# Optimization experiments

Measured on AMD Instinct MI355X. Metric: run time of the kernel, lower is better.

## Reference

```python
import jax, jax.numpy as jnp
import numpy as np

B, Q, V, H, U = 4, 256, 2048, 512, 128

def setup_inputs() -> dict:
    key = jax.random.key(0)
    ks = jax.random.split(key, 5)
    return {
        "queries": jax.random.normal(ks[0], (B, Q, H), dtype=jnp.float32),
        "values": jax.random.normal(ks[1], (B, V, H), dtype=jnp.float32),
        "w1": jax.random.normal(ks[2], (H, U), dtype=jnp.float32) / np.sqrt(H),
        "w2": jax.random.normal(ks[3], (H, U), dtype=jnp.float32) / np.sqrt(H),
        "v": jax.random.normal(ks[4], (U,), dtype=jnp.float32) / np.sqrt(U),
    }

def reference(queries, values, w1, w2, v):
    # Project queries and values first (cheap GEMMs), then broadcast-add.
    pq = jnp.einsum("bqh,hu->bqu", queries, w1)          # [B,Q,U]
    pv = jnp.einsum("bvh,hu->bvu", values, w2)           # [B,V,U]
    # added_qv: [B,Q,V,U] -- the large intermediate the original materializes
    scores = jnp.einsum("bqvu,u->bqv", jnp.tanh(pq[:, :, None, :] + pv[:, None, :, :]), v)
    attn = jax.nn.softmax(scores, axis=-1)               # softmax over V (last axis, as tf.nn.softmax)
    return jnp.einsum("bqv,bvh->bqh", attn, values)      # [B,Q,H]
```

## Files before the change

kernel.cpp:

```cpp
#include <hip/hip_runtime.h>

#define BB 4
#define QQ 256
#define VV 2048
#define HH 512
#define UU 128

#define C2E   2.8853900817779268f
#define LOG2E 1.4426950408889634f

__device__ __forceinline__ void fma4(float4& a, float s, const float4& w) {
    a.x = fmaf(s, w.x, a.x);
    a.y = fmaf(s, w.y, a.y);
    a.z = fmaf(s, w.z, a.z);
    a.w = fmaf(s, w.w, a.w);
}
__device__ __forceinline__ float2 rcp2(float2 x) {
    return make_float2(__builtin_amdgcn_rcpf(x.x), __builtin_amdgcn_rcpf(x.y));
}
__device__ __forceinline__ float2 mul2(float2 a, float2 b) { return make_float2(a.x*b.x, a.y*b.y); }
__device__ __forceinline__ float2 muls(float2 a, float s)  { return make_float2(a.x*s, a.y*s); }
__device__ __forceinline__ float2 fma2(float2 a, float2 b, float2 c) {
    return make_float2(fmaf(a.x, b.x, c.x), fmaf(a.y, b.y, c.y));
}
__device__ __forceinline__ float2 fmas(float2 a, float s, float2 c) {
    return make_float2(fmaf(a.x, s, c.x), fmaf(a.y, s, c.y));
}

__global__ __launch_bounds__(256) void proj_kernel(const float* __restrict__ queries,
                                                   const float* __restrict__ values,
                                                   const float* __restrict__ w1,
                                                   const float* __restrict__ w2,
                                                   float* __restrict__ pqI,
                                                   float* __restrict__ pvI,
                                                   float* __restrict__ denom) {
    __shared__ float smem[32 * 36 + 32 * 128];
    float (*As)[36] = (float(*)[36])smem;
    float* Ws = smem + 32 * 36;
    float (*Ls)[36] = (float(*)[36])smem;

    const int bid = blockIdx.x;
    const int tid = threadIdx.x;
    if (bid == 0) *(float4*)&denom[tid * 4] = make_float4(0.f, 0.f, 0.f, 0.f);

    const bool isv = (bid < 256);
    const float* A; const float* W; int b, r0, ROWS; float* Ob;
    if (isv) {
        b = bid >> 6; r0 = (bid & 63) * 32;
        A = values + ((size_t)(b * VV + r0)) * HH;  W = w2;
        Ob = pvI + (size_t)b * UU * VV;  ROWS = VV;
    } else {
        const int q = bid - 256;
        b = q >> 3; r0 = (q & 7) * 32;
        A = queries + ((size_t)(b * QQ + r0)) * HH; W = w1;
        Ob = pqI + (size_t)b * UU * QQ;  ROWS = QQ;
    }

    const int tx = tid & 31;
    const int ty = tid >> 5;
    float4 acc[4];
#pragma unroll
    for (int j = 0; j < 4; j++) acc[j] = make_float4(0.f, 0.f, 0.f, 0.f);

    for (int k0 = 0; k0 < HH; k0 += 32) {
        {
            const int r = tid >> 3, kk4 = (tid & 7) * 4;
            const float4 a = *(const float4*)&A[(size_t)r * HH + k0 + kk4];
            As[kk4 + 0][r] = a.x; As[kk4 + 1][r] = a.y;
            As[kk4 + 2][r] = a.z; As[kk4 + 3][r] = a.w;
        }
#pragma unroll
        for (int t = 0; t < 4; t++) {
            const int f = tid + t * 256;
            const int kk = f >> 5, u4 = (f & 31) * 4;
            *(float4*)&Ws[kk * 128 + u4] = *(const float4*)&W[(size_t)(k0 + kk) * UU + u4];
        }
        __syncthreads();
#pragma unroll
        for (int kk = 0; kk < 32; kk++) {
            const float4 a = *(const float4*)&As[kk][ty * 4];
            const float4 w = *(const float4*)&Ws[kk * 128 + tx * 4];
            fma4(acc[0], a.x, w);
            fma4(acc[1], a.y, w);
            fma4(acc[2], a.z, w);
            fma4(acc[3], a.w, w);
        }
        __syncthreads();
    }
#pragma unroll
    for (int j = 0; j < 4; j++) {
        const float aa[4] = {acc[j].x, acc[j].y, acc[j].z, acc[j].w};
#pragma unroll
        for (int i = 0; i < 4; i++)
            Ls[tx * 4 + i][ty * 4 + j] = __builtin_amdgcn_exp2f(aa[i] * C2E);
    }
    __syncthreads();
#pragma unroll
    for (int t = 0; t < 4; t++) {
        const int idx = tid + t * 256;
        const int g = idx >> 5, r = idx & 31;
        float4 o;
        o.x = Ls[4 * g + 0][r]; o.y = Ls[4 * g + 1][r];
        o.z = Ls[4 * g + 2][r]; o.w = Ls[4 * g + 3][r];
        *(float4*)&Ob[((size_t)g * ROWS + r0 + r) * 4] = o;
    }
}

__global__ __launch_bounds__(1024, 8) void fused_kernel(const float* __restrict__ pqI,
                                                        const float* __restrict__ pvI,
                                                        const float* __restrict__ vvec,
                                                        const float* __restrict__ values,
                                                        float* __restrict__ slab,
                                                        float* __restrict__ denom) {
    __shared__ float att[512][20];
    __shared__ float scratch[24 * 512];
    __shared__ float wred[8][16];
    __shared__ float eqs[32 * 64];
    const int tid = threadIdx.x;
    const int bid = blockIdx.x;
    const int vs = bid & 3, qb = (bid >> 2) & 15, b = bid >> 6;
    const int qbase = qb * 16, vbase = vs * 512;

    const int vloc = tid & 511;
    const int uh = tid >> 9;
    const int v = vbase + vloc;

    const float* pv4 = pvI + (size_t)b * UU * VV + (size_t)v * 4;
    const float* pq4 = pqI + (size_t)b * UU * QQ + (size_t)qbase * 4;

    if (tid < 512) {
        const int G = tid >> 4, f4 = tid & 15;
        *(float4*)&eqs[G * 64 + f4 * 4] = *(const float4*)&pq4[(size_t)G * QQ * 4 + f4 * 4];
    }

    float vsum = 0.0f;
#pragma unroll
    for (int u4 = 0; u4 < UU; u4 += 4) {
        const float4 t = *(const float4*)&vvec[u4];
        vsum += t.x + t.y + t.z + t.w;
    }

    float2 acc[8];
#pragma unroll
    for (int p = 0; p < 8; p++) acc[p] = make_float2(0.f, 0.f);

    const int G0 = uh * 16;
    float4 ev = *(const float4*)&pv4[(size_t)G0 * VV * 4];
    __syncthreads();

    for (int g = 0; g < 16; g++) {
        const int G = G0 + g;
        const float* eqp = &eqs[G * 64];
        float4 evn;
        if (g < 15) evn = *(const float4*)&pv4[(size_t)(G + 1) * VV * 4];
        const float4 wq = *(const float4*)&vvec[G * 4];
        const float w0 = 2.f * wq.x, w1 = 2.f * wq.y;
        const float w2 = 2.f * wq.z, w3 = 2.f * wq.w;
#pragma unroll
        for (int p = 0; p < 8; p++) {
            const float4 e0 = *(const float4*)&eqp[(2 * p) * 4];
            const float4 e1 = *(const float4*)&eqp[(2 * p + 1) * 4];
            const float2 a1 = make_float2(fmaf(e0.x, ev.x, 1.f), fmaf(e1.x, ev.x, 1.f));
            const float2 b1 = make_float2(fmaf(e0.y, ev.y, 1.f), fmaf(e1.y, ev.y, 1.f));
            const float2 c1 = make_float2(fmaf(e0.z, ev.z, 1.f), fmaf(e1.z, ev.z, 1.f));
            const float2 d1 = make_float2(fmaf(e0.w, ev.w, 1.f), fmaf(e1.w, ev.w, 1.f));
            const float2 pab = mul2(a1, b1), pcd = mul2(c1, d1);
            const float2 nab = fmas(a1, w1, muls(b1, w0));
            const float2 ncd = fmas(c1, w3, muls(d1, w2));
            const float2 num = fma2(nab, pcd, mul2(ncd, pab));
            const float2 den = mul2(pab, pcd);
            acc[p] = fma2(num, rcp2(den), acc[p]);
        }
        ev = evn;
    }

    float* cb = scratch;
    if (uh == 1) {
#pragma unroll
        for (int p = 0; p < 8; p++) {
            cb[(2 * p + 0) * 512 + vloc] = acc[p].x;
            cb[(2 * p + 1) * 512 + vloc] = acc[p].y;
        }
    }
    __syncthreads();
    if (uh == 0) {
#pragma unroll
        for (int p = 0; p < 8; p++) {
            const float hx = cb[(2 * p + 0) * 512 + vloc];
            const float hy = cb[(2 * p + 1) * 512 + vloc];
            float2 e;
            e.x = __builtin_amdgcn_exp2f((vsum - (acc[p].x + hx)) * LOG2E);
            e.y = __builtin_amdgcn_exp2f((vsum - (acc[p].y + hy)) * LOG2E);
            *(float2*)&att[vloc][2 * p] = e;
            acc[p] = e;
        }
#pragma unroll
        for (int off = 1; off < 64; off <<= 1) {
#pragma unroll
            for (int p = 0; p < 8; p++) {
                acc[p].x += __shfl_xor(acc[p].x, off, 64);
                acc[p].y += __shfl_xor(acc[p].y, off, 64);
            }
        }
        if ((tid & 63) == 0) {
            const int w = tid >> 6;
#pragma unroll
            for (int p = 0; p < 8; p++) {
                wred[w][2 * p + 0] = acc[p].x;
                wred[w][2 * p + 1] = acc[p].y;
            }
        }
    }
    __syncthreads();
    if (tid < 16) {
        float s = 0.f;
#pragma unroll
        for (int w = 0; w < 8; w++) s += wred[w][tid];
        atomicAdd(&denom[b * QQ + qbase + tid], s);
    }

    const int hg = tid & 127, sel = tid >> 7;
    const int qh = sel & 1, vh = sel >> 1;
    const int h0 = hg * 4;
    const float* vp = values + ((size_t)(b * VV + vbase + vh * 128)) * HH + h0;

    float4 oacc[8];
#pragma unroll
    for (int j = 0; j < 8; j++) oacc[j] = make_float4(0.f, 0.f, 0.f, 0.f);

#pragma unroll 2
    for (int vv = 0; vv < 128; vv++) {
        const float4 w = *(const float4*)&vp[(size_t)vv * HH];
        const float4 a0 = *(const float4*)&att[vh * 128 + vv][qh * 8 + 0];
        const float4 a1 = *(const float4*)&att[vh * 128 + vv][qh * 8 + 4];
        fma4(oacc[0], a0.x, w); fma4(oacc[1], a0.y, w);
        fma4(oacc[2], a0.z, w); fma4(oacc[3], a0.w, w);
        fma4(oacc[4], a1.x, w); fma4(oacc[5], a1.y, w);
        fma4(oacc[6], a1.z, w); fma4(oacc[7], a1.w, w);
    }

    float (*scr)[512] = (float(*)[512])scratch;
    for (int rr = 0; rr < 2; rr++) {
        __syncthreads();
        if (qh == rr && vh > 0) {
#pragma unroll
            for (int j = 0; j < 8; j++)
                *(float4*)&scr[(vh - 1) * 8 + j][h0] = oacc[j];
        }
        __syncthreads();
        if (qh == rr && vh == 0) {
            float* sp = slab + (size_t)vs * (BB * QQ * HH);
#pragma unroll
            for (int j = 0; j < 8; j++) {
                const float4 p0 = *(const float4*)&scr[0 * 8 + j][h0];
                const float4 p1 = *(const float4*)&scr[1 * 8 + j][h0];
                const float4 p2 = *(const float4*)&scr[2 * 8 + j][h0];
                float4 o;
                o.x = oacc[j].x + p0.x + p1.x + p2.x;
                o.y = oacc[j].y + p0.y + p1.y + p2.y;
                o.z = oacc[j].z + p0.z + p1.z + p2.z;
                o.w = oacc[j].w + p0.w + p1.w + p2.w;
                *(float4*)&sp[((size_t)(b * QQ + qbase + rr * 8 + j)) * HH + h0] = o;
            }
        }
    }
}

__global__ __launch_bounds__(256) void reduce_kernel(const float* __restrict__ slab,
                                                     const float* __restrict__ denom,
                                                     float* __restrict__ out) {
    const int i = blockIdx.x * 256 + threadIdx.x;
    const float r = __builtin_amdgcn_rcpf(denom[i >> 7]);
    const float4* s4 = (const float4*)slab;
    float4 s = s4[i];
#pragma unroll
    for (int k = 1; k < 4; k++) {
        const float4 p = s4[(size_t)k * (BB * QQ * HH / 4) + i];
        s.x += p.x; s.y += p.y; s.z += p.z; s.w += p.w;
    }
    s.x *= r; s.y *= r; s.z *= r; s.w *= r;
    ((float4*)out)[i] = s;
}

extern "C" void kernel_launch(void* const* d_in, const int* in_sizes, int n_in,
                              void* d_out, int out_size, void* d_ws, size_t ws_size,
                              hipStream_t stream) {
    const float* queries = (const float*)d_in[0];
    const float* values  = (const float*)d_in[1];
    const float* w1      = (const float*)d_in[2];
    const float* w2      = (const float*)d_in[3];
    const float* vvec    = (const float*)d_in[4];
    float* out = (float*)d_out;

    float* ws    = (float*)d_ws;
    float* pqI   = ws;
    float* pvI   = pqI + BB * UU * QQ;
    float* denom = pvI + (size_t)BB * UU * VV;
    float* slab  = denom + BB * QQ;

    proj_kernel<<<256 + 32, 256, 0, stream>>>(queries, values, w1, w2, pqI, pvI, denom);
    fused_kernel<<<BB * (QQ / 16) * (VV / 512), 1024, 0, stream>>>(pqI, pvI, vvec, values, slab, denom);
    reduce_kernel<<<(BB * QQ * HH) / 4 / 256, 256, 0, stream>>>(slab, denom, out);
}
```

Baseline: 166.8 us.

## Use split-bf16 MFMA for attention-values GEMM with transposed bf16 values

The projection kernel now also writes a transposed copy of values, split into high and low bf16 halves. The fused kernel stores the softmax weights as hi/lo bf16 in LDS. It then computes the attn×values product with 16x16x32 bf16 MFMA instructions using three products per tile (hh, lh, hl) in place of scalar FP32 FMAs. This moves the final GEMM onto matrix cores while keeping near-FP32 accuracy. The cost is extra global writes and reads of the two bf16 planes, and strided 2-byte stores in the projection kernel.

Result: slower. 170.2 us (+2.0%).

```diff
diff --git a/kernel.cpp b/kernel.cpp
--- a/kernel.cpp
+++ b/kernel.cpp
@@ -9,6 +9,10 @@
 #define C2E   2.8853900817779268f
 #define LOG2E 1.4426950408889634f
 
+typedef unsigned short u16;
+typedef __attribute__((ext_vector_type(8))) short bf16x8;
+typedef __attribute__((ext_vector_type(4))) float f32x4;
+
 __device__ __forceinline__ void fma4(float4& a, float s, const float4& w) {
     a.x = fmaf(s, w.x, a.x);
     a.y = fmaf(s, w.y, a.y);
@@ -25,6 +29,12 @@
 }
 __device__ __forceinline__ float2 fmas(float2 a, float s, float2 c) {
     return make_float2(fmaf(a.x, s, c.x), fmaf(a.y, s, c.y));
+}
+__device__ __forceinline__ void bsplit(float x, u16& h, u16& l) {
+    const unsigned bx = __float_as_uint(x);
+    h = (u16)(bx >> 16);
+    const float lo = x - __uint_as_float(bx & 0xFFFF0000u);
+    l = (u16)(__float_as_uint(lo) >> 16);
 }
 
 __global__ __launch_bounds__(256) void proj_kernel(const float* __restrict__ queries,
@@ -33,7 +43,9 @@
                                                    const float* __restrict__ w2,
                                                    float* __restrict__ pqI,
                                                    float* __restrict__ pvI,
-                                                   float* __restrict__ denom) {
+                                                   float* __restrict__ denom,
+                                                   u16* __restrict__ vTh,
+                                                   u16* __restrict__ vTl) {
     __shared__ float smem[32 * 36 + 32 * 128];
     float (*As)[36] = (float(*)[36])smem;
     float* Ws = smem + 32 * 36;
@@ -85,6 +97,17 @@
             fma4(acc[2], a.z, w);
             fma4(acc[3], a.w, w);
         }
+        if (isv) {
+#pragma unroll
+            for (int t = 0; t < 4; t++) {
+                const int kk = (tid >> 5) + 8 * t;
+                const int r  = tid & 31;
+                u16 h16, l16;
+                bsplit(As[kk][r], h16, l16);
+                const size_t o = ((size_t)b * HH + k0 + kk) * VV + r0 + r;
+                vTh[o] = h16; vTl[o] = l16;
+            }
+        }
         __syncthreads();
     }
 #pragma unroll
@@ -109,11 +132,13 @@
 __global__ __launch_bounds__(1024, 8) void fused_kernel(const float* __restrict__ pqI,
                                                         const float* __restrict__ pvI,
                                                         const float* __restrict__ vvec,
-                                                        const float* __restrict__ values,
+                                                        const u16* __restrict__ vTh,
+                                                        const u16* __restrict__ vTl,
                                                         float* __restrict__ slab,
                                                         float* __restrict__ denom) {
-    __shared__ float att[512][20];
-    __shared__ float scratch[24 * 512];
+    __shared__ __attribute__((aligned(16))) u16 attH[16 * 520];
+    __shared__ __attribute__((aligned(16))) u16 attL[16 * 520];
+    __shared__ float scratch[16 * 512];
     __shared__ float wred[8][16];
     __shared__ float eqs[32 * 64];
     const int tid = threadIdx.x;
@@ -191,7 +216,11 @@
             float2 e;
             e.x = __builtin_amdgcn_exp2f((vsum - (acc[p].x + hx)) * LOG2E);
             e.y = __builtin_amdgcn_exp2f((vsum - (acc[p].y + hy)) * LOG2E);
-            *(float2*)&att[vloc][2 * p] = e;
+            u16 hh, ll;
+            bsplit(e.x, hh, ll);
+            attH[(2 * p + 0) * 520 + vloc] = hh; attL[(2 * p + 0) * 520 + vloc] = ll;
+            bsplit(e.y, hh, ll);
+            attH[(2 * p + 1) * 520 + vloc] = hh; attL[(2 * p + 1) * 520 + vloc] = ll;
             acc[p] = e;
         }
 #pragma unroll
@@ -219,50 +248,36 @@
         atomicAdd(&denom[b * QQ + qbase + tid], s);
     }
 
-    const int hg = tid & 127, sel = tid >> 7;
-    const int qh = sel & 1, vh = sel >> 1;
-    const int h0 = hg * 4;
-    const float* vp = values + ((size_t)(b * VV + vbase + vh * 128)) * HH + h0;
-
-    float4 oacc[8];
-#pragma unroll
-    for (int j = 0; j < 8; j++) oacc[j] = make_float4(0.f, 0.f, 0.f, 0.f);
-
-#pragma unroll 2
-    for (int vv = 0; vv < 128; vv++) {
-        const float4 w = *(const float4*)&vp[(size_t)vv * HH];
-        const float4 a0 = *(const float4*)&att[vh * 128 + vv][qh * 8 + 0];
-        const float4 a1 = *(const float4*)&att[vh * 128 + vv][qh * 8 + 4];
-        fma4(oacc[0], a0.x, w); fma4(oacc[1], a0.y, w);
-        fma4(oacc[2], a0.z, w); fma4(oacc[3], a0.w, w);
-        fma4(oacc[4], a1.x, w); fma4(oacc[5], a1.y, w);
-        fma4(oacc[6], a1.z, w); fma4(oacc[7], a1.w, w);
-    }
-
-    float (*scr)[512] = (float(*)[512])scratch;
-    for (int rr = 0; rr < 2; rr++) {
-        __syncthreads();
-        if (qh == rr && vh > 0) {
-#pragma unroll
-            for (int j = 0; j < 8; j++)
-                *(float4*)&scr[(vh - 1) * 8 + j][h0] = oacc[j];
-        }
-        __syncthreads();
-        if (qh == rr && vh == 0) {
-            float* sp = slab + (size_t)vs * (BB * QQ * HH);
-#pragma unroll
-            for (int j = 0; j < 8; j++) {
-                const float4 p0 = *(const float4*)&scr[0 * 8 + j][h0];
-                const float4 p1 = *(const float4*)&scr[1 * 8 + j][h0];
-                const float4 p2 = *(const float4*)&scr[2 * 8 + j][h0];
-                float4 o;
-                o.x = oacc[j].x + p0.x + p1.x + p2.x;
-                o.y = oacc[j].y + p0.y + p1.y + p2.y;
-                o.z = oacc[j].z + p0.z + p1.z + p2.z;
-                o.w = oacc[j].w + p0.w + p1.w + p2.w;
-                *(float4*)&sp[((size_t)(b * QQ + qbase + rr * 8 + j)) * HH + h0] = o;
-            }
-        }
+    const int ln = tid & 63, wv = tid >> 6;
+    const int m = ln & 15, g4 = ln >> 4;
+    const int h0 = wv * 32;
+    const u16* vtH0 = vTh + ((size_t)(b * HH + h0 + m)) * VV + vbase;
+    const u16* vtL0 = vTl + ((size_t)(b * HH + h0 + m)) * VV + vbase;
+    const u16* vtH1 = vtH0 + (size_t)16 * VV;
+    const u16* vtL1 = vtL0 + (size_t)16 * VV;
+
+    f32x4 acc0 = {0.f, 0.f, 0.f, 0.f}, acc1 = {0.f, 0.f, 0.f, 0.f};
+#pragma unroll 4
+    for (int kk = 0; kk < 16; kk++) {
+        const int vk = kk * 32 + g4 * 8;
+        const bf16x8 aH = *(const bf16x8*)&attH[m * 520 + vk];
+        const bf16x8 aL = *(const bf16x8*)&attL[m * 520 + vk];
+        const bf16x8 bH0 = *(const bf16x8*)&vtH0[vk];
+        const bf16x8 bL0 = *(const bf16x8*)&vtL0[vk];
+        const bf16x8 bH1 = *(const bf16x8*)&vtH1[vk];
+        const bf16x8 bL1 = *(const bf16x8*)&vtL1[vk];
+        acc0 = __builtin_amdgcn_mfma_f32_16x16x32_bf16(aH, bH0, acc0, 0, 0, 0);
+        acc1 = __builtin_amdgcn_mfma_f32_16x16x32_bf16(aH, bH1, acc1, 0, 0, 0);
+        acc0 = __builtin_amdgcn_mfma_f32_16x16x32_bf16(aL, bH0, acc0, 0, 0, 0);
+        acc1 = __builtin_amdgcn_mfma_f32_16x16x32_bf16(aL, bH1, acc1, 0, 0, 0);
+        acc0 = __builtin_amdgcn_mfma_f32_16x16x32_bf16(aH, bL0, acc0, 0, 0, 0);
+        acc1 = __builtin_amdgcn_mfma_f32_16x16x32_bf16(aH, bL1, acc1, 0, 0, 0);
+    }
+    float* sp = slab + (size_t)vs * (BB * QQ * HH) + ((size_t)(b * QQ + qbase)) * HH;
+#pragma unroll
+    for (int i = 0; i < 4; i++) {
+        sp[(size_t)(g4 * 4 + i) * HH + h0 + m]      = acc0[i];
+        sp[(size_t)(g4 * 4 + i) * HH + h0 + 16 + m] = acc1[i];
     }
 }
 
@@ -297,8 +312,10 @@
     float* pvI   = pqI + BB * UU * QQ;
     float* denom = pvI + (size_t)BB * UU * VV;
     float* slab  = denom + BB * QQ;
-
-    proj_kernel<<<256 + 32, 256, 0, stream>>>(queries, values, w1, w2, pqI, pvI, denom);
-    fused_kernel<<<BB * (QQ / 16) * (VV / 512), 1024, 0, stream>>>(pqI, pvI, vvec, values, slab, denom);
+    u16*   vTh   = (u16*)(slab + (size_t)4 * BB * QQ * HH);
+    u16*   vTl   = vTh + (size_t)BB * HH * VV;
+
+    proj_kernel<<<256 + 32, 256, 0, stream>>>(queries, values, w1, w2, pqI, pvI, denom, vTh, vTl);
+    fused_kernel<<<BB * (QQ / 16) * (VV / 512), 1024, 0, stream>>>(pqI, pvI, vvec, vTh, vTl, slab, denom);
     reduce_kernel<<<(BB * QQ * HH) / 4 / 256, 256, 0, stream>>>(slab, denom, out);
 }
```

## Retile score phase so each thread covers 4 values by 4 queries

Applied to the files above, without the earlier changes.

The score computation changes from each thread handling one value position across all 16 queries to each thread handling 4 value positions across a 4-query slice. The wave reduction for the softmax denominator shrinks accordingly, and launch bounds move from 8 to 4 waves per EU, giving the compiler more registers. The aim is fewer LDS reads of the query projections per value, more independent work per thread, and less shuffle traffic. In exchange, each thread issues four strided global loads of pv per step, and the block may run at lower occupancy.

New measurement: 162.8 us. -2.4%, faster.

```diff
diff --git a/kernel.cpp b/kernel.cpp
--- a/kernel.cpp
+++ b/kernel.cpp
@@ -106,7 +106,7 @@
     }
 }
 
-__global__ __launch_bounds__(1024, 8) void fused_kernel(const float* __restrict__ pqI,
+__global__ __launch_bounds__(1024, 4) void fused_kernel(const float* __restrict__ pqI,
                                                         const float* __restrict__ pvI,
                                                         const float* __restrict__ vvec,
                                                         const float* __restrict__ values,
@@ -114,18 +114,17 @@
                                                         float* __restrict__ denom) {
     __shared__ float att[512][20];
     __shared__ float scratch[24 * 512];
-    __shared__ float wred[8][16];
+    __shared__ float wred[8][8];
     __shared__ float eqs[32 * 64];
     const int tid = threadIdx.x;
     const int bid = blockIdx.x;
     const int vs = bid & 3, qb = (bid >> 2) & 15, b = bid >> 6;
     const int qbase = qb * 16, vbase = vs * 512;
 
-    const int vloc = tid & 511;
+    const int vgrp = tid & 127;
+    const int qq = (tid >> 7) & 3;
     const int uh = tid >> 9;
-    const int v = vbase + vloc;
-
-    const float* pv4 = pvI + (size_t)b * UU * VV + (size_t)v * 4;
+
     const float* pq4 = pqI + (size_t)b * UU * QQ + (size_t)qbase * 4;
 
     if (tid < 512) {
@@ -140,87 +139,108 @@
         vsum += t.x + t.y + t.z + t.w;
     }
 
-    float2 acc[8];
-#pragma unroll
-    for (int p = 0; p < 8; p++) acc[p] = make_float2(0.f, 0.f);
+    const float* pvb = pvI + (size_t)b * UU * VV + (size_t)(vbase + vgrp) * 4;
+
+    float2 acc[4][2];
+#pragma unroll
+    for (int k = 0; k < 4; k++) { acc[k][0] = make_float2(0.f, 0.f); acc[k][1] = make_float2(0.f, 0.f); }
 
     const int G0 = uh * 16;
-    float4 ev = *(const float4*)&pv4[(size_t)G0 * VV * 4];
+    float4 ev[4], evn[4];
+#pragma unroll
+    for (int k = 0; k < 4; k++)
+        ev[k] = *(const float4*)&pvb[(size_t)G0 * VV * 4 + k * 128 * 4];
     __syncthreads();
 
     for (int g = 0; g < 16; g++) {
         const int G = G0 + g;
-        const float* eqp = &eqs[G * 64];
-        float4 evn;
-        if (g < 15) evn = *(const float4*)&pv4[(size_t)(G + 1) * VV * 4];
+        const float* eqp = &eqs[G * 64 + qq * 16];
+        if (g < 15) {
+#pragma unroll
+            for (int k = 0; k < 4; k++)
+                evn[k] = *(const float4*)&pvb[(size_t)(G + 1) * VV * 4 + k * 128 * 4];
+        }
         const float4 wq = *(const float4*)&vvec[G * 4];
         const float w0 = 2.f * wq.x, w1 = 2.f * wq.y;
         const float w2 = 2.f * wq.z, w3 = 2.f * wq.w;
 #pragma unroll
-        for (int p = 0; p < 8; p++) {
+        for (int p = 0; p < 2; p++) {
             const float4 e0 = *(const float4*)&eqp[(2 * p) * 4];
             const float4 e1 = *(const float4*)&eqp[(2 * p + 1) * 4];
-            const float2 a1 = make_float2(fmaf(e0.x, ev.x, 1.f), fmaf(e1.x, ev.x, 1.f));
-            const float2 b1 = make_float2(fmaf(e0.y, ev.y, 1.f), fmaf(e1.y, ev.y, 1.f));
-            const float2 c1 = make_float2(fmaf(e0.z, ev.z, 1.f), fmaf(e1.z, ev.z, 1.f));
-            const float2 d1 = make_float2(fmaf(e0.w, ev.w, 1.f), fmaf(e1.w, ev.w, 1.f));
-            const float2 pab = mul2(a1, b1), pcd = mul2(c1, d1);
-            const float2 nab = fmas(a1, w1, muls(b1, w0));
-            const float2 ncd = fmas(c1, w3, muls(d1, w2));
-            const float2 num = fma2(nab, pcd, mul2(ncd, pab));
-            const float2 den = mul2(pab, pcd);
-            acc[p] = fma2(num, rcp2(den), acc[p]);
-        }
-        ev = evn;
+#pragma unroll
+            for (int k = 0; k < 4; k++) {
+                const float2 a1 = make_float2(fmaf(e0.x, ev[k].x, 1.f), fmaf(e1.x, ev[k].x, 1.f));
+                const float2 b1 = make_float2(fmaf(e0.y, ev[k].y, 1.f), fmaf(e1.y, ev[k].y, 1.f));
+                const float2 c1 = make_float2(fmaf(e0.z, ev[k].z, 1.f), fmaf(e1.z, ev[k].z, 1.f));
+                const float2 d1 = make_float2(fmaf(e0.w, ev[k].w, 1.f), fmaf(e1.w, ev[k].w, 1.f));
+                const float2 pab = mul2(a1, b1), pcd = mul2(c1, d1);
+                const float2 nab = fmas(a1, w1, muls(b1, w0));
+                const float2 ncd = fmas(c1, w3, muls(d1, w2));
+                const float2 num = fma2(nab, pcd, mul2(ncd, pab));
+                const float2 den = mul2(pab, pcd);
+                acc[k][p] = fma2(num, rcp2(den), acc[k][p]);
+            }
+        }
+#pragma unroll
+        for (int k = 0; k < 4; k++) ev[k] = evn[k];
     }
 
     float* cb = scratch;
     if (uh == 1) {
 #pragma unroll
-        for (int p = 0; p < 8; p++) {
-            cb[(2 * p + 0) * 512 + vloc] = acc[p].x;
-            cb[(2 * p + 1) * 512 + vloc] = acc[p].y;
-        }
+        for (int p = 0; p < 2; p++)
+#pragma unroll
+            for (int k = 0; k < 4; k++) {
+                cb[(qq * 4 + 2 * p + 0) * 512 + vgrp + k * 128] = acc[k][p].x;
+                cb[(qq * 4 + 2 * p + 1) * 512 + vgrp + k * 128] = acc[k][p].y;
+            }
     }
     __syncthreads();
     if (uh == 0) {
 #pragma unroll
-        for (int p = 0; p < 8; p++) {
-            const float hx = cb[(2 * p + 0) * 512 + vloc];
-            const float hy = cb[(2 * p + 1) * 512 + vloc];
-            float2 e;
-            e.x = __builtin_amdgcn_exp2f((vsum - (acc[p].x + hx)) * LOG2E);
-            e.y = __builtin_amdgcn_exp2f((vsum - (acc[p].y + hy)) * LOG2E);
-            *(float2*)&att[vloc][2 * p] = e;
-            acc[p] = e;
+        for (int p = 0; p < 2; p++)
+#pragma unroll
+            for (int k = 0; k < 4; k++) {
+                const float hx = cb[(qq * 4 + 2 * p + 0) * 512 + vgrp + k * 128];
+                const float hy = cb[(qq * 4 + 2 * p + 1) * 512 + vgrp + k * 128];
+                float2 e;
+                e.x = __builtin_amdgcn_exp2f((vsum - (acc[k][p].x + hx)) * LOG2E);
+                e.y = __builtin_amdgcn_exp2f((vsum - (acc[k][p].y + hy)) * LOG2E);
+                *(float2*)&att[vgrp + k * 128][qq * 4 + 2 * p] = e;
+                acc[k][p] = e;
+            }
+        float2 s[2];
+#pragma unroll
+        for (int p = 0; p < 2; p++) {
+            s[p].x = acc[0][p].x + acc[1][p].x + acc[2][p].x + acc[3][p].x;
+            s[p].y = acc[0][p].y + acc[1][p].y + acc[2][p].y + acc[3][p].y;
         }
 #pragma unroll
         for (int off = 1; off < 64; off <<= 1) {
 #pragma unroll
-            for (int p = 0; p < 8; p++) {
-                acc[p].x += __shfl_xor(acc[p].x, off, 64);
-                acc[p].y += __shfl_xor(acc[p].y, off, 64);
+            for (int p = 0; p < 2; p++) {
+                s[p].x += __shfl_xor(s[p].x, off, 64);
+                s[p].y += __shfl_xor(s[p].y, off, 64);
             }
         }
         if ((tid & 63) == 0) {
             const int w = tid >> 6;
 #pragma unroll
-            for (int p = 0; p < 8; p++) {
-                wred[w][2 * p + 0] = acc[p].x;
-                wred[w][2 * p + 1] = acc[p].y;
+            for (int p = 0; p < 2; p++) {
+                wred[w][2 * p + 0] = s[p].x;
+                wred[w][2 * p + 1] = s[p].y;
             }
         }
     }
     __syncthreads();
     if (tid < 16) {
-        float s = 0.f;
-#pragma unroll
-        for (int w = 0; w < 8; w++) s += wred[w][tid];
-        atomicAdd(&denom[b * QQ + qbase + tid], s);
+        const int qq2 = tid >> 2, j = tid & 3;
+        atomicAdd(&denom[b * QQ + qbase + tid],
+                  wred[2 * qq2][j] + wred[2 * qq2 + 1][j]);
     }
 
     const int hg = tid & 127, sel = tid >> 7;
-    const int qh = sel & 1, vh = sel >> 1;
+    const int qhb = sel & 1, vh = sel >> 1;
     const int h0 = hg * 4;
     const float* vp = values + ((size_t)(b * VV + vbase + vh * 128)) * HH + h0;
 
@@ -231,8 +251,8 @@
 #pragma unroll 2
     for (int vv = 0; vv < 128; vv++) {
         const float4 w = *(const float4*)&vp[(size_t)vv * HH];
-        const float4 a0 = *(const float4*)&att[vh * 128 + vv][qh * 8 + 0];
-        const float4 a1 = *(const float4*)&att[vh * 128 + vv][qh * 8 + 4];
+        const float4 a0 = *(const float4*)&att[vh * 128 + vv][qhb * 8 + 0];
+        const float4 a1 = *(const float4*)&att[vh * 128 + vv][qhb * 8 + 4];
         fma4(oacc[0], a0.x, w); fma4(oacc[1], a0.y, w);
         fma4(oacc[2], a0.z, w); fma4(oacc[3], a0.w, w);
         fma4(oacc[4], a1.x, w); fma4(oacc[5], a1.y, w);
@@ -242,13 +262,13 @@
     float (*scr)[512] = (float(*)[512])scratch;
     for (int rr = 0; rr < 2; rr++) {
         __syncthreads();
-        if (qh == rr && vh > 0) {
+        if (qhb == rr && vh > 0) {
 #pragma unroll
             for (int j = 0; j < 8; j++)
                 *(float4*)&scr[(vh - 1) * 8 + j][h0] = oacc[j];
         }
         __syncthreads();
-        if (qh == rr && vh == 0) {
+        if (qhb == rr && vh == 0) {
             float* sp = slab + (size_t)vs * (BB * QQ * HH);
 #pragma unroll
             for (int j = 0; j < 8; j++) {
```
